# Kernel optimization log

Hardware: AMD Instinct MI355X
Metric: run time of the kernel (lower is better)

Reference implementation:

```python
import jax, jax.numpy as jnp
import numpy as np

K = 16
ITERS = 5
DIST_CHUNK = 8  # feature-chunk size to avoid materializing [B,F,S,S]


def pairwise_l1(x):
    """x: [B, F, S] -> d: [B, S, S], d[b,i,j] = ||x[b,:,i]-x[b,:,j]||_1.
    Computed in feature chunks via scan so peak intermediate is [B,CH,S,S]."""
    B, F, S = x.shape
    xc = x.reshape(B, F // DIST_CHUNK, DIST_CHUNK, S).transpose(1, 0, 2, 3)  # [F/CH,B,CH,S]

    def step(acc, blk):  # blk: [B, CH, S]
        return acc + jnp.abs(blk[:, :, :, None] - blk[:, :, None, :]).sum(axis=1), None

    d, _ = jax.lax.scan(step, jnp.zeros((B, S, S), x.dtype), xc)
    return d


def kmedoids_pool(x, w):
    B, F, S = x.shape
    wm = jnp.mean(w, axis=1)                       # [B,S] per-token attention weight
    d = pairwise_l1(x)                             # [B,S,S]
    _, ctr = jax.lax.top_k(wm, K)                  # [B,K] initial medoids
    dw = d * wm[:, None, :]                        # d[b,i,j]*w[b,j]
    for _ in range(ITERS):
        # distance from every token to each current medoid: [B,S,K]
        i2c = jnp.take_along_axis(d, jnp.broadcast_to(ctr[:, None, :], (B, S, K)), axis=2)
        assign = jnp.argmin(i2c, axis=2)           # [B,S] cluster assignment
        member = jax.nn.one_hot(assign, K, dtype=x.dtype)  # [B,S,K]
        # weighted within-cluster cost for candidate i in cluster k:
        # cost[b,i,k] = sum_j d[b,i,j]*w[b,j]*member[b,j,k]
        cost = jnp.einsum('bij,bjk->bik', dw, member)
        cost = jnp.where(member > 0, cost, jnp.inf)  # medoid must be a member
        ctr = jnp.argmin(cost, axis=1)             # [B,K] new medoids
    idx = jnp.broadcast_to(ctr[:, None, :], (B, F, K))
    return jnp.take_along_axis(x, idx, axis=2)     # [B,F,K]


def setup_inputs() -> dict:
    key = jax.random.key(0)
    kx, kw = jax.random.split(key)
    B, F, S = 8, 256, 1024
    x = jax.random.normal(kx, (B, F, S), dtype=jnp.float32)
    w = jax.random.uniform(kw, (B, S, S), dtype=jnp.float32)
    return {"x": x, "w": w}


def reference(x, w):
    return kmedoids_pool(x, w)
```

## Files before the change

### kernel.cpp

```cpp
#include <hip/hip_runtime.h>
#include <math.h>

#define BB 8
#define FF 256
#define SS 1024
#define KK 16
#define ITERS 5

typedef unsigned long long ull;

#define ICH 8
__global__ void wm_part_kernel(const float* __restrict__ w, float* __restrict__ part) {
    int j = blockIdx.x * 256 + threadIdx.x;
    int ic = blockIdx.y, b = blockIdx.z;
    const float* wp = w + (size_t)b * SS * SS + (size_t)ic * (SS / ICH) * SS + j;
    float s = 0.f;
#pragma unroll 8
    for (int i = 0; i < SS / ICH; ++i) s += wp[(size_t)i * SS];
    part[((size_t)ic * BB + b) * SS + j] = s;
}

__global__ void wm_final_kernel(const float* __restrict__ part, float* __restrict__ wm) {
    int t = blockIdx.x * blockDim.x + threadIdx.x;
    if (t >= BB * SS) return;
    int b = t / SS, j = t % SS;
    float s = 0.f;
#pragma unroll
    for (int ic = 0; ic < ICH; ++ic) s += part[((size_t)ic * BB + b) * SS + j];
    wm[t] = s * (1.0f / SS);
}

#define FC 32
__device__ __forceinline__ void async_copy16(const float* g, const float* s) {
    __builtin_amdgcn_global_load_lds((const __attribute__((address_space(1))) void*)g,
                                     (__attribute__((address_space(3))) void*)s, 16, 0, 0);
}

__global__ __launch_bounds__(256) void dist_kernel(const float* __restrict__ x,
                                                   float* __restrict__ d) {
    __shared__ float smem[4 * 3072];
    int tid = threadIdx.x;
    int wave = tid >> 6, lane = tid & 63;
    int b = blockIdx.y;
    int w = blockIdx.x * 4 + wave;
    int it = 0, rem = w;
    while (rem >= 32 - 2 * it) { rem -= 32 - 2 * it; ++it; }
    int jt = 2 * it + rem;
    int i0 = it * 64, j0 = jt * 32;

    float* As = smem + wave * 3072;
    float* Bs = As + 2048;
    const float* xb = x + (size_t)b * FF * SS;
    float* db = d + (size_t)b * SS * SS;
    int ly = lane >> 3, lx = lane & 7;
    int aFl = lane >> 4, aTk = (lane & 15) * 4;
    int bFl = lane >> 3, bTk = (lane & 7) * 4;

    float acc[8][4] = {};
    for (int f0 = 0; f0 < FF; f0 += FC) {
        asm volatile("s_waitcnt lgkmcnt(0)" ::: "memory");
#pragma unroll
        for (int c = 0; c < 8; ++c)
            async_copy16(xb + (size_t)(f0 + c * 4 + aFl) * SS + i0 + aTk, As + c * 256);
#pragma unroll
        for (int c = 0; c < 4; ++c)
            async_copy16(xb + (size_t)(f0 + c * 8 + bFl) * SS + j0 + bTk, Bs + c * 256);
        asm volatile("s_waitcnt vmcnt(0)" ::: "memory");
#pragma unroll 4
        for (int f = 0; f < FC; ++f) {
            const float* af = As + f * 64 + ly * 8;
            const float* bf = Bs + f * 32 + lx * 4;
            float4 a0 = *(const float4*)af;
            float4 a1 = *(const float4*)(af + 4);
            float4 bb = *(const float4*)bf;
            float av[8] = {a0.x, a0.y, a0.z, a0.w, a1.x, a1.y, a1.z, a1.w};
            float bv[4] = {bb.x, bb.y, bb.z, bb.w};
#pragma unroll
            for (int r = 0; r < 8; ++r)
#pragma unroll
                for (int c = 0; c < 4; ++c)
                    acc[r][c] += fabsf(av[r] - bv[c]);
        }
    }
#pragma unroll
    for (int r = 0; r < 8; ++r) {
        float4 v = make_float4(acc[r][0], acc[r][1], acc[r][2], acc[r][3]);
        *(float4*)&db[(size_t)(i0 + ly * 8 + r) * SS + j0 + lx * 4] = v;
    }
    if (rem >= 2) {
#pragma unroll
        for (int c = 0; c < 4; ++c) {
            float4 lo = make_float4(acc[0][c], acc[1][c], acc[2][c], acc[3][c]);
            float4 hi = make_float4(acc[4][c], acc[5][c], acc[6][c], acc[7][c]);
            float* p = &db[(size_t)(j0 + lx * 4 + c) * SS + i0 + ly * 8];
            *(float4*)p = lo;
            *(float4*)(p + 4) = hi;
        }
    }
}

__global__ __launch_bounds__(1024) void topk_assign_kernel(const float* __restrict__ wm,
                                                           const float* __restrict__ d,
                                                           int* __restrict__ assign) {
    int b = blockIdx.x;
    int tid = threadIdx.x;
    int lane = tid & 63, wv = tid >> 6;
    __shared__ ull red[16];
    __shared__ int ctr_s[KK];
    float v = wm[b * SS + tid];
    ull key = (((ull)__float_as_uint(v)) << 32) | (ull)(0xFFFFFFFFu - (unsigned)tid);
    for (int k = 0; k < KK; ++k) {
        ull kk = key;
#pragma unroll
        for (int off = 32; off; off >>= 1) {
            ull o = __shfl_down(kk, off, 64);
            if (o > kk) kk = o;
        }
        if (lane == 0) red[wv] = kk;
        __syncthreads();
        if (wv == 0) {
            ull k2 = (lane < 16) ? red[lane] : 0ull;
#pragma unroll
            for (int off = 8; off; off >>= 1) {
                ull o = __shfl_down(k2, off, 64);
                if (o > k2) k2 = o;
            }
            if (lane == 0) red[0] = k2;
        }
        __syncthreads();
        ull W = red[0];
        int widx = (int)(0xFFFFFFFFu - (unsigned)(W & 0xFFFFFFFFu));
        if (tid == widx) key = 0;
        if (tid == 0) ctr_s[k] = widx;
        __syncthreads();
    }
    const float* db = d + (size_t)b * SS * SS;
    float bv = INFINITY;
    int bk = 0;
#pragma unroll
    for (int k = 0; k < KK; ++k) {
        float vv = db[(size_t)ctr_s[k] * SS + tid];
        if (vv < bv) { bv = vv; bk = k; }
    }
    assign[b * SS + tid] = bk;
}

__global__ __launch_bounds__(256) void cost_kernel(const float* __restrict__ d,
                                                   const float* __restrict__ wm,
                                                   const int* __restrict__ assign,
                                                   float* __restrict__ cost) {
    int b = blockIdx.y;
    int i = blockIdx.x;
    int tid = threadIdx.x;
    int my = assign[b * SS + i];
    const float* drow = d + (size_t)b * SS * SS + (size_t)i * SS;
    const float* wb = wm + b * SS;
    const int* ab = assign + b * SS;
    float4 dv = *(const float4*)&drow[tid * 4];
    float4 wv = *(const float4*)&wb[tid * 4];
    int4 av = *(const int4*)&ab[tid * 4];
    float s = 0.f;
    s += (av.x == my) ? dv.x * wv.x : 0.f;
    s += (av.y == my) ? dv.y * wv.y : 0.f;
    s += (av.z == my) ? dv.z * wv.z : 0.f;
    s += (av.w == my) ? dv.w * wv.w : 0.f;
#pragma unroll
    for (int off = 32; off > 0; off >>= 1) s += __shfl_down(s, off, 64);
    __shared__ float ws_s[4];
    if ((tid & 63) == 0) ws_s[tid >> 6] = s;
    __syncthreads();
    if (tid == 0) cost[b * SS + i] = (ws_s[0] + ws_s[1]) + (ws_s[2] + ws_s[3]);
}

__global__ __launch_bounds__(1024) void update_assign_kernel(
        const float* __restrict__ d, const float* __restrict__ cost,
        int* __restrict__ assign, const float* __restrict__ x,
        float* __restrict__ out, int last) {
    int b = blockIdx.x;
    int tid = threadIdx.x;
    int lane = tid & 63, wv = tid >> 6;
    __shared__ float cost_s[SS];
    __shared__ int assign_s[SS];
    __shared__ int ctr_s[KK];
    cost_s[tid] = cost[b * SS + tid];
    assign_s[tid] = assign[b * SS + tid];
    __syncthreads();
    ull best = ~0ull;
    int k = wv;
    for (int c = 0; c < SS / 64; ++c) {
        int i = c * 64 + lane;
        if (assign_s[i] == k) {
            ull key = (((ull)__float_as_uint(cost_s[i])) << 32) | (unsigned)i;
            if (key < best) best = key;
        }
    }
#pragma unroll
    for (int off = 32; off; off >>= 1) {
        ull o = __shfl_down(best, off, 64);
        if (o < best) best = o;
    }
    if (lane == 0) ctr_s[k] = (best == ~0ull) ? 0 : (int)(best & 0xFFFFFFFFu);
    __syncthreads();
    if (!last) {
        const float* db = d + (size_t)b * SS * SS;
        float bv = INFINITY;
        int bk = 0;
#pragma unroll
        for (int k2 = 0; k2 < KK; ++k2) {
            float vv = db[(size_t)ctr_s[k2] * SS + tid];
            if (vv < bv) { bv = vv; bk = k2; }
        }
        assign[b * SS + tid] = bk;
    } else {
        for (int e = tid; e < FF * KK; e += 1024) {
            int f = e / KK, k2 = e % KK;
            out[((size_t)b * FF + f) * KK + k2] = x[((size_t)b * FF + f) * SS + ctr_s[k2]];
        }
    }
}

extern "C" void kernel_launch(void* const* d_in, const int* in_sizes, int n_in,
                              void* d_out, int out_size, void* d_ws, size_t ws_size,
                              hipStream_t stream) {
    const float* x = (const float*)d_in[0];
    const float* w = (const float*)d_in[1];
    float* out = (float*)d_out;

    char* ws = (char*)d_ws;
    float* d = (float*)ws;
    size_t off = (size_t)BB * SS * SS * sizeof(float);
    float* wm = (float*)(ws + off);  off += (size_t)BB * SS * sizeof(float);
    int* assign = (int*)(ws + off);  off += (size_t)BB * SS * sizeof(int);
    float* cost = (float*)(ws + off);
    float* part = (float*)ws;

    wm_part_kernel<<<dim3(SS / 256, ICH, BB), 256, 0, stream>>>(w, part);
    wm_final_kernel<<<(BB * SS + 255) / 256, 256, 0, stream>>>(part, wm);
    dist_kernel<<<dim3(68, BB), 256, 0, stream>>>(x, d);
    topk_assign_kernel<<<BB, 1024, 0, stream>>>(wm, d, assign);
    for (int itr = 0; itr < ITERS; ++itr) {
        cost_kernel<<<dim3(SS, BB), 256, 0, stream>>>(d, wm, assign, cost);
        update_assign_kernel<<<BB, 1024, 0, stream>>>(d, cost, assign, x, out,
                                                      itr == ITERS - 1 ? 1 : 0);
    }
}
```

Baseline: 256.1 us.

## Double-buffer distance kernel loads and fold medoid argmin into cost via atomics

The distance kernel becomes one wave per block with a double-buffered async global-to-LDS pipeline over 16-feature chunks, so loads for the next chunk overlap compute on the current one. The per-cluster argmin over candidate costs moves into the cost kernel as a 64-bit atomicMin on a packed (cost, index) key, which removes the serial 8-block update kernel. A separate wider assignment kernel and a gather kernel replace it. Exchanges are more atomics, a per-iteration ctr buffer that must be initialised in topk, and smaller blocks with launch-bounds occupancy hints.

```diff
diff --git a/kernel.cpp b/kernel.cpp
--- a/kernel.cpp
+++ b/kernel.cpp
@@ -30,26 +30,22 @@
     wm[t] = s * (1.0f / SS);
 }
 
-#define FC 32
+#define FCD 16
 __device__ __forceinline__ void async_copy16(const float* g, const float* s) {
     __builtin_amdgcn_global_load_lds((const __attribute__((address_space(1))) void*)g,
                                      (__attribute__((address_space(3))) void*)s, 16, 0, 0);
 }
 
-__global__ __launch_bounds__(256) void dist_kernel(const float* __restrict__ x,
-                                                   float* __restrict__ d) {
-    __shared__ float smem[4 * 3072];
-    int tid = threadIdx.x;
-    int wave = tid >> 6, lane = tid & 63;
+__global__ __launch_bounds__(64, 4) void dist_kernel(const float* __restrict__ x,
+                                                     float* __restrict__ d) {
+    __shared__ float smem[3072];
+    int lane = threadIdx.x;
     int b = blockIdx.y;
-    int w = blockIdx.x * 4 + wave;
+    int w = blockIdx.x;
     int it = 0, rem = w;
     while (rem >= 32 - 2 * it) { rem -= 32 - 2 * it; ++it; }
     int jt = 2 * it + rem;
     int i0 = it * 64, j0 = jt * 32;
-
-    float* As = smem + wave * 3072;
-    float* Bs = As + 2048;
     const float* xb = x + (size_t)b * FF * SS;
     float* db = d + (size_t)b * SS * SS;
     int ly = lane >> 3, lx = lane & 7;
@@ -57,19 +53,25 @@
     int bFl = lane >> 3, bTk = (lane & 7) * 4;
 
     float acc[8][4] = {};
-    for (int f0 = 0; f0 < FF; f0 += FC) {
-        asm volatile("s_waitcnt lgkmcnt(0)" ::: "memory");
-#pragma unroll
-        for (int c = 0; c < 8; ++c)
-            async_copy16(xb + (size_t)(f0 + c * 4 + aFl) * SS + i0 + aTk, As + c * 256);
-#pragma unroll
-        for (int c = 0; c < 4; ++c)
-            async_copy16(xb + (size_t)(f0 + c * 8 + bFl) * SS + j0 + bTk, Bs + c * 256);
-        asm volatile("s_waitcnt vmcnt(0)" ::: "memory");
+
+    auto stage = [&](int c, int h) {
+        float* A = smem + h * 1536;
+        float* B = A + 1024;
+        const float* base = xb + (size_t)c * FCD * SS;
+#pragma unroll
+        for (int ci = 0; ci < 4; ++ci)
+            async_copy16(base + (size_t)(ci * 4 + aFl) * SS + i0 + aTk, A + ci * 256);
+#pragma unroll
+        for (int ci = 0; ci < 2; ++ci)
+            async_copy16(base + (size_t)(ci * 8 + bFl) * SS + j0 + bTk, B + ci * 256);
+    };
+    auto compute = [&](int h) {
+        const float* A = smem + h * 1536;
+        const float* B = A + 1024;
 #pragma unroll 4
-        for (int f = 0; f < FC; ++f) {
-            const float* af = As + f * 64 + ly * 8;
-            const float* bf = Bs + f * 32 + lx * 4;
+        for (int f = 0; f < FCD; ++f) {
+            const float* af = A + f * 64 + ly * 8;
+            const float* bf = B + f * 32 + lx * 4;
             float4 a0 = *(const float4*)af;
             float4 a1 = *(const float4*)(af + 4);
             float4 bb = *(const float4*)bf;
@@ -81,7 +83,19 @@
                 for (int c = 0; c < 4; ++c)
                     acc[r][c] += fabsf(av[r] - bv[c]);
         }
-    }
+    };
+
+    stage(0, 0);
+#pragma unroll 1
+    for (int k = 0; k < FF / FCD - 1; ++k) {
+        asm volatile("s_waitcnt lgkmcnt(0)" ::: "memory");
+        stage(k + 1, (k + 1) & 1);
+        asm volatile("s_waitcnt vmcnt(6)" ::: "memory");
+        compute(k & 1);
+    }
+    asm volatile("s_waitcnt vmcnt(0)" ::: "memory");
+    compute(1);
+
 #pragma unroll
     for (int r = 0; r < 8; ++r) {
         float4 v = make_float4(acc[r][0], acc[r][1], acc[r][2], acc[r][3]);
@@ -101,10 +115,12 @@
 
 __global__ __launch_bounds__(1024) void topk_assign_kernel(const float* __restrict__ wm,
                                                            const float* __restrict__ d,
-                                                           int* __restrict__ assign) {
+                                                           int* __restrict__ assign,
+                                                           ull* __restrict__ ctrbuf) {
     int b = blockIdx.x;
     int tid = threadIdx.x;
     int lane = tid & 63, wv = tid >> 6;
+    if (tid < ITERS * KK) ctrbuf[(tid / KK) * BB * KK + b * KK + (tid % KK)] = ~0ull;
     __shared__ ull red[16];
     __shared__ int ctr_s[KK];
     float v = wm[b * SS + tid];
@@ -148,7 +164,7 @@
 __global__ __launch_bounds__(256) void cost_kernel(const float* __restrict__ d,
                                                    const float* __restrict__ wm,
                                                    const int* __restrict__ assign,
-                                                   float* __restrict__ cost) {
+                                                   ull* __restrict__ ctrn) {
     int b = blockIdx.y;
     int i = blockIdx.x;
     int tid = threadIdx.x;
@@ -169,54 +185,41 @@
     __shared__ float ws_s[4];
     if ((tid & 63) == 0) ws_s[tid >> 6] = s;
     __syncthreads();
-    if (tid == 0) cost[b * SS + i] = (ws_s[0] + ws_s[1]) + (ws_s[2] + ws_s[3]);
-}
-
-__global__ __launch_bounds__(1024) void update_assign_kernel(
-        const float* __restrict__ d, const float* __restrict__ cost,
-        int* __restrict__ assign, const float* __restrict__ x,
-        float* __restrict__ out, int last) {
-    int b = blockIdx.x;
-    int tid = threadIdx.x;
-    int lane = tid & 63, wv = tid >> 6;
-    __shared__ float cost_s[SS];
-    __shared__ int assign_s[SS];
-    __shared__ int ctr_s[KK];
-    cost_s[tid] = cost[b * SS + tid];
-    assign_s[tid] = assign[b * SS + tid];
-    __syncthreads();
-    ull best = ~0ull;
-    int k = wv;
-    for (int c = 0; c < SS / 64; ++c) {
-        int i = c * 64 + lane;
-        if (assign_s[i] == k) {
-            ull key = (((ull)__float_as_uint(cost_s[i])) << 32) | (unsigned)i;
-            if (key < best) best = key;
-        }
-    }
-#pragma unroll
-    for (int off = 32; off; off >>= 1) {
-        ull o = __shfl_down(best, off, 64);
-        if (o < best) best = o;
-    }
-    if (lane == 0) ctr_s[k] = (best == ~0ull) ? 0 : (int)(best & 0xFFFFFFFFu);
-    __syncthreads();
-    if (!last) {
-        const float* db = d + (size_t)b * SS * SS;
-        float bv = INFINITY;
-        int bk = 0;
-#pragma unroll
-        for (int k2 = 0; k2 < KK; ++k2) {
-            float vv = db[(size_t)ctr_s[k2] * SS + tid];
-            if (vv < bv) { bv = vv; bk = k2; }
-        }
-        assign[b * SS + tid] = bk;
-    } else {
-        for (int e = tid; e < FF * KK; e += 1024) {
-            int f = e / KK, k2 = e % KK;
-            out[((size_t)b * FF + f) * KK + k2] = x[((size_t)b * FF + f) * SS + ctr_s[k2]];
-        }
-    }
+    if (tid == 0) {
+        float c = (ws_s[0] + ws_s[1]) + (ws_s[2] + ws_s[3]);
+        ull key = (((ull)__float_as_uint(c)) << 32) | (unsigned)i;
+        atomicMin(&ctrn[b * KK + my], key);
+    }
+}
+
+__global__ __launch_bounds__(256) void assign_from_kernel(const float* __restrict__ d,
+                                                          const ull* __restrict__ ctrn,
+                                                          int* __restrict__ assign) {
+    int b = blockIdx.y;
+    int i = blockIdx.x * 256 + threadIdx.x;
+    const float* db = d + (size_t)b * SS * SS;
+    float bv = INFINITY;
+    int bk = 0;
+#pragma unroll
+    for (int k = 0; k < KK; ++k) {
+        ull key = ctrn[b * KK + k];
+        int c = (key == ~0ull) ? 0 : (int)(key & 0xFFFFFFFFu);
+        float vv = db[(size_t)c * SS + i];
+        if (vv < bv) { bv = vv; bk = k; }
+    }
+    assign[b * SS + i] = bk;
+}
+
+__global__ void gather_kernel(const float* __restrict__ x, const ull* __restrict__ ctrn,
+                              float* __restrict__ out) {
+    int t = blockIdx.x * blockDim.x + threadIdx.x;
+    if (t >= BB * FF * KK) return;
+    int b = t / (FF * KK);
+    int f = (t / KK) % FF;
+    int k = t % KK;
+    ull key = ctrn[b * KK + k];
+    int c = (key == ~0ull) ? 0 : (int)(key & 0xFFFFFFFFu);
+    out[t] = x[(size_t)b * FF * SS + (size_t)f * SS + c];
 }
 
 extern "C" void kernel_launch(void* const* d_in, const int* in_sizes, int n_in,
@@ -231,16 +234,20 @@
     size_t off = (size_t)BB * SS * SS * sizeof(float);
     float* wm = (float*)(ws + off);  off += (size_t)BB * SS * sizeof(float);
     int* assign = (int*)(ws + off);  off += (size_t)BB * SS * sizeof(int);
-    float* cost = (float*)(ws + off);
+    off = (off + 15) & ~(size_t)15;
+    ull* ctrbuf = (ull*)(ws + off);
     float* part = (float*)ws;
 
     wm_part_kernel<<<dim3(SS / 256, ICH, BB), 256, 0, stream>>>(w, part);
     wm_final_kernel<<<(BB * SS + 255) / 256, 256, 0, stream>>>(part, wm);
-    dist_kernel<<<dim3(68, BB), 256, 0, stream>>>(x, d);
-    topk_assign_kernel<<<BB, 1024, 0, stream>>>(wm, d, assign);
+    dist_kernel<<<dim3(272, BB), 64, 0, stream>>>(x, d);
+    topk_assign_kernel<<<BB, 1024, 0, stream>>>(wm, d, assign, ctrbuf);
     for (int itr = 0; itr < ITERS; ++itr) {
-        cost_kernel<<<dim3(SS, BB), 256, 0, stream>>>(d, wm, assign, cost);
-        update_assign_kernel<<<BB, 1024, 0, stream>>>(d, cost, assign, x, out,
-                                                      itr == ITERS - 1 ? 1 : 0);
-    }
-}
+        ull* ctrn = ctrbuf + (size_t)itr * BB * KK;
+        cost_kernel<<<dim3(SS, BB), 256, 0, stream>>>(d, wm, assign, ctrn);
+        if (itr < ITERS - 1)
+            assign_from_kernel<<<dim3(SS / 256, BB), 256, 0, stream>>>(d, ctrn, assign);
+        else
+            gather_kernel<<<(BB * FF * KK + 255) / 256, 256, 0, stream>>>(x, ctrn, out);
+    }
+}
```

Measured after the change: 327.6 us. +27.9%, slower.

## Restructure distance kernel to single-wave 32x32 tiles with double-buffered async loads

Applied to the files above, without the earlier changes.

The pairwise L1 distance kernel moves from 4-wave blocks computing 64x32 tiles to single-wave blocks computing 32x32 tiles over the upper triangle, launched as 528 blocks per batch. Feature chunks shrink to 16 and are double-buffered in LDS, so the async global-to-LDS copy of the next chunk overlaps with computing the current one. The intent is more parallelism and latency hiding than the old load-then-compute loop. In exchange, smaller tiles lower arithmetic intensity per load, and there are more blocks and more triangle-indexing overhead.

```diff
diff --git a/kernel.cpp b/kernel.cpp
--- a/kernel.cpp
+++ b/kernel.cpp
@@ -30,71 +30,77 @@
     wm[t] = s * (1.0f / SS);
 }
 
-#define FC 32
+#define FCD 16
 __device__ __forceinline__ void async_copy16(const float* g, const float* s) {
     __builtin_amdgcn_global_load_lds((const __attribute__((address_space(1))) void*)g,
                                      (__attribute__((address_space(3))) void*)s, 16, 0, 0);
 }
 
-__global__ __launch_bounds__(256) void dist_kernel(const float* __restrict__ x,
-                                                   float* __restrict__ d) {
-    __shared__ float smem[4 * 3072];
-    int tid = threadIdx.x;
-    int wave = tid >> 6, lane = tid & 63;
+__global__ __launch_bounds__(64, 4) void dist_kernel(const float* __restrict__ x,
+                                                     float* __restrict__ d) {
+    __shared__ float smem[2048];
+    int lane = threadIdx.x;
     int b = blockIdx.y;
-    int w = blockIdx.x * 4 + wave;
+    int w = blockIdx.x;
     int it = 0, rem = w;
-    while (rem >= 32 - 2 * it) { rem -= 32 - 2 * it; ++it; }
-    int jt = 2 * it + rem;
-    int i0 = it * 64, j0 = jt * 32;
-
-    float* As = smem + wave * 3072;
-    float* Bs = As + 2048;
+    while (rem >= 32 - it) { rem -= 32 - it; ++it; }
+    int jt = it + rem;
+    int i0 = it * 32, j0 = jt * 32;
     const float* xb = x + (size_t)b * FF * SS;
     float* db = d + (size_t)b * SS * SS;
     int ly = lane >> 3, lx = lane & 7;
-    int aFl = lane >> 4, aTk = (lane & 15) * 4;
-    int bFl = lane >> 3, bTk = (lane & 7) * 4;
-
-    float acc[8][4] = {};
-    for (int f0 = 0; f0 < FF; f0 += FC) {
-        asm volatile("s_waitcnt lgkmcnt(0)" ::: "memory");
-#pragma unroll
-        for (int c = 0; c < 8; ++c)
-            async_copy16(xb + (size_t)(f0 + c * 4 + aFl) * SS + i0 + aTk, As + c * 256);
-#pragma unroll
-        for (int c = 0; c < 4; ++c)
-            async_copy16(xb + (size_t)(f0 + c * 8 + bFl) * SS + j0 + bTk, Bs + c * 256);
-        asm volatile("s_waitcnt vmcnt(0)" ::: "memory");
+    int sFl = lane >> 3, sTk = (lane & 7) * 4;
+
+    float acc[4][4] = {};
+
+    auto stage = [&](int c, int h) {
+        float* A = smem + h * 1024;
+        float* B = A + 512;
+        const float* base = xb + (size_t)c * FCD * SS;
+#pragma unroll
+        for (int ci = 0; ci < 2; ++ci) {
+            async_copy16(base + (size_t)(ci * 8 + sFl) * SS + i0 + sTk, A + ci * 256);
+            async_copy16(base + (size_t)(ci * 8 + sFl) * SS + j0 + sTk, B + ci * 256);
+        }
+    };
+    auto compute = [&](int h) {
+        const float* A = smem + h * 1024;
+        const float* B = A + 512;
 #pragma unroll 4
-        for (int f = 0; f < FC; ++f) {
-            const float* af = As + f * 64 + ly * 8;
-            const float* bf = Bs + f * 32 + lx * 4;
-            float4 a0 = *(const float4*)af;
-            float4 a1 = *(const float4*)(af + 4);
-            float4 bb = *(const float4*)bf;
-            float av[8] = {a0.x, a0.y, a0.z, a0.w, a1.x, a1.y, a1.z, a1.w};
+        for (int f = 0; f < FCD; ++f) {
+            float4 a = *(const float4*)(A + f * 32 + ly * 4);
+            float4 bb = *(const float4*)(B + f * 32 + lx * 4);
+            float av[4] = {a.x, a.y, a.z, a.w};
             float bv[4] = {bb.x, bb.y, bb.z, bb.w};
 #pragma unroll
-            for (int r = 0; r < 8; ++r)
+            for (int r = 0; r < 4; ++r)
 #pragma unroll
                 for (int c = 0; c < 4; ++c)
                     acc[r][c] += fabsf(av[r] - bv[c]);
         }
-    }
-#pragma unroll
-    for (int r = 0; r < 8; ++r) {
+    };
+
+    stage(0, 0);
+#pragma unroll 1
+    for (int k = 0; k < FF / FCD - 1; ++k) {
+        asm volatile("s_waitcnt lgkmcnt(0)" ::: "memory");
+        stage(k + 1, (k + 1) & 1);
+        asm volatile("s_waitcnt vmcnt(4)" ::: "memory");
+        compute(k & 1);
+    }
+    asm volatile("s_waitcnt vmcnt(0)" ::: "memory");
+    compute(1);
+
+#pragma unroll
+    for (int r = 0; r < 4; ++r) {
         float4 v = make_float4(acc[r][0], acc[r][1], acc[r][2], acc[r][3]);
-        *(float4*)&db[(size_t)(i0 + ly * 8 + r) * SS + j0 + lx * 4] = v;
-    }
-    if (rem >= 2) {
+        *(float4*)&db[(size_t)(i0 + ly * 4 + r) * SS + j0 + lx * 4] = v;
+    }
+    if (it != jt) {
 #pragma unroll
         for (int c = 0; c < 4; ++c) {
-            float4 lo = make_float4(acc[0][c], acc[1][c], acc[2][c], acc[3][c]);
-            float4 hi = make_float4(acc[4][c], acc[5][c], acc[6][c], acc[7][c]);
-            float* p = &db[(size_t)(j0 + lx * 4 + c) * SS + i0 + ly * 8];
-            *(float4*)p = lo;
-            *(float4*)(p + 4) = hi;
+            float4 v = make_float4(acc[0][c], acc[1][c], acc[2][c], acc[3][c]);
+            *(float4*)&db[(size_t)(j0 + lx * 4 + c) * SS + i0 + ly * 4] = v;
         }
     }
 }
@@ -236,7 +242,7 @@
 
     wm_part_kernel<<<dim3(SS / 256, ICH, BB), 256, 0, stream>>>(w, part);
     wm_final_kernel<<<(BB * SS + 255) / 256, 256, 0, stream>>>(part, wm);
-    dist_kernel<<<dim3(68, BB), 256, 0, stream>>>(x, d);
+    dist_kernel<<<dim3(528, BB), 64, 0, stream>>>(x, d);
     topk_assign_kernel<<<BB, 1024, 0, stream>>>(wm, d, assign);
     for (int itr = 0; itr < ITERS; ++itr) {
         cost_kernel<<<dim3(SS, BB), 256, 0, stream>>>(d, wm, assign, cost);
```

New measurement: 240.3 us. 1.07x faster.
